# Optimization experiments

Hardware: AMD Instinct MI355X
Metric: run time of the kernel (lower is better)

The kernel has to match this reference:

```python
import jax, jax.numpy as jnp
import numpy as np

EPS = 1e-5  # torch GroupNorm default


def setup_inputs() -> dict:
    key = jax.random.key(0)
    ks = jax.random.split(key, 7)
    B, H, W, C = 8, 64, 64, 64
    x = jax.random.normal(ks[0], (B, H, W, C), dtype=jnp.float32)
    temb = jax.random.normal(ks[1], (B, 256), dtype=jnp.float32)
    scale = 0.02
    Wq = jax.random.normal(ks[2], (C, C), dtype=jnp.float32) * scale
    Wk = jax.random.normal(ks[3], (C, C), dtype=jnp.float32) * scale
    Wv = jax.random.normal(ks[4], (C, C), dtype=jnp.float32) * scale
    Wo = jax.random.normal(ks[5], (C, C), dtype=jnp.float32) * scale
    z = jnp.zeros((C,), dtype=jnp.float32)
    return {"x": x, "temb": temb, "Wq": Wq, "bq": z, "Wk": Wk, "bk": z,
            "Wv": Wv, "bv": z, "Wo": Wo, "bo": z}


def reference(x, temb, Wq, bq, Wk, bk, Wv, bv, Wo, bo):
    # x: [B, H, W, C] channels-last. temb is accepted but unused (as in source).
    B, H, W, C = x.shape
    S = H * W
    # normalize(): freshly-built GroupNorm(num_groups=1) with identity affine
    # -> standardize over all non-batch dims.
    mu = jnp.mean(x, axis=(1, 2, 3), keepdims=True)
    var = jnp.var(x, axis=(1, 2, 3), keepdims=True)
    h = (x - mu) * jax.lax.rsqrt(var + EPS)
    hf = h.reshape(B, S, C)
    q = hf @ Wq.T + bq  # [B, S, C]
    k = hf @ Wk.T + bk
    v = hf @ Wv.T + bv
    # full (S x S) score matrix, scaled by C^-0.5, naive softmax
    w = jnp.einsum('bsc,btc->bst', q, k) * (C ** -0.5)
    w = jax.nn.softmax(w, axis=-1)
    o = jnp.einsum('bst,btc->bsc', w, v)  # [B, S, C]
    o = o @ Wo.T + bo
    return x + o.reshape(B, H, W, C)
```

## Files before the change

### kernel.cpp

```cpp
#include <hip/hip_runtime.h>
#include <hip/hip_bf16.h>
#include <math.h>

#define B_ 8
#define S_ 4096
#define C_ 64
#define EPSV 1e-5f

using floatx4  = __attribute__((ext_vector_type(4)))  float;
using floatx16 = __attribute__((ext_vector_type(16))) float;
using bf16x8   = __attribute__((ext_vector_type(8)))  short;

typedef __attribute__((address_space(3))) unsigned int       as3_u32;
typedef __attribute__((address_space(1))) const unsigned int as1_u32;

__device__ __forceinline__ short f2bf(float f) {
    unsigned u = __builtin_bit_cast(unsigned, f);
    u = u + 0x7fffu + ((u >> 16) & 1u);
    return (short)(u >> 16);
}

__device__ __forceinline__ float bf2f(short s) {
    return __builtin_bit_cast(float, ((unsigned)(unsigned short)s) << 16);
}

__device__ __forceinline__ unsigned cvt_pk_bf16(float lo, float hi) {
    unsigned r;
    asm volatile("v_cvt_pk_bf16_f32 %0, %1, %2" : "=v"(r) : "v"(lo), "v"(hi));
    return r;
}

__device__ __forceinline__ void perm32swap(unsigned &a, unsigned &b) {
#if __has_builtin(__builtin_amdgcn_permlane32_swap)
    auto r = __builtin_amdgcn_permlane32_swap((int)a, (int)b, false, false);
    a = (unsigned)r[0];
    b = (unsigned)r[1];
#else
    asm volatile("v_permlane32_swap_b32 %0, %1" : "+v"(a), "+v"(b));
#endif
}

__device__ __forceinline__ bf16x8 ld_w_frag(const float* __restrict__ W, int n, int kk, int g, int c) {
    const float* p = W + (16 * n + c) * C_ + 32 * kk + 8 * g;
    bf16x8 r;
#pragma unroll
    for (int j = 0; j < 8; ++j) r[j] = f2bf(p[j]);
    return r;
}

__global__ __launch_bounds__(256) void stats1_kernel(const float* __restrict__ x,
                                                     float* __restrict__ partial) {
    int b = blockIdx.x >> 5, chunk = blockIdx.x & 31;
    const float4* xb = (const float4*)x + (size_t)b * 65536 + chunk * 2048;
    float s = 0.f, ss = 0.f;
#pragma unroll
    for (int i = 0; i < 8; ++i) {
        float4 v = xb[threadIdx.x + i * 256];
        s  += v.x + v.y + v.z + v.w;
        ss += v.x * v.x + v.y * v.y + v.z * v.z + v.w * v.w;
    }
    for (int off = 32; off > 0; off >>= 1) {
        s  += __shfl_down(s, off);
        ss += __shfl_down(ss, off);
    }
    __shared__ float sm[4], ssm[4];
    int wid = threadIdx.x >> 6, lane = threadIdx.x & 63;
    if (lane == 0) { sm[wid] = s; ssm[wid] = ss; }
    __syncthreads();
    if (threadIdx.x == 0) {
        partial[blockIdx.x * 2]     = sm[0] + sm[1] + sm[2] + sm[3];
        partial[blockIdx.x * 2 + 1] = ssm[0] + ssm[1] + ssm[2] + ssm[3];
    }
}

__global__ __launch_bounds__(512) void stats2_kernel(const float* __restrict__ partial,
                                                     float* __restrict__ stats) {
    int w = threadIdx.x >> 6, lane = threadIdx.x & 63;
    float s = 0.f, ss = 0.f;
    if (lane < 32) {
        s  = partial[(w * 32 + lane) * 2];
        ss = partial[(w * 32 + lane) * 2 + 1];
    }
    for (int off = 16; off > 0; off >>= 1) {
        s  += __shfl_down(s, off);
        ss += __shfl_down(ss, off);
    }
    if (lane == 0) {
        const float invN = 1.0f / (float)(S_ * C_);
        float mu  = s * invN;
        float var = ss * invN - mu * mu;
        stats[w * 2]     = mu;
        stats[w * 2 + 1] = rsqrtf(var + EPSV);
    }
}

__global__ __launch_bounds__(256) void proj_kernel(
    const float* __restrict__ x,
    const float* __restrict__ Wq, const float* __restrict__ bq,
    const float* __restrict__ Wk, const float* __restrict__ bk,
    const float* __restrict__ Wv, const float* __restrict__ bv,
    const float* __restrict__ stats,
    short* __restrict__ qo, char* __restrict__ kws, char* __restrict__ vws) {
    __shared__ char hbuf[64 * 128];

    int b  = blockIdx.x >> 6;
    int t_ = blockIdx.x & 63;
    int s0 = t_ * 64;
    float mu = stats[b * 2], rs = stats[b * 2 + 1];
    const float* xt = x + ((size_t)b * S_ + s0) * C_;
    int t = threadIdx.x;

#pragma unroll
    for (int i = 0; i < 4; ++i) {
        int fi  = t + 256 * i;
        int row = fi >> 4;
        int c4  = fi & 15;
        float4 v = *(const float4*)(xt + row * C_ + c4 * 4);
        unsigned lo = (unsigned)(unsigned short)f2bf((v.x - mu) * rs) |
                      ((unsigned)(unsigned short)f2bf((v.y - mu) * rs) << 16);
        unsigned hi = (unsigned)(unsigned short)f2bf((v.z - mu) * rs) |
                      ((unsigned)(unsigned short)f2bf((v.w - mu) * rs) << 16);
        int off = row * 128 + c4 * 8;
        off ^= (row & 7) << 4;
        *(uint2*)(hbuf + off) = make_uint2(lo, hi);
    }
    __syncthreads();

    int lane = t & 63, w = t >> 6;
    int g = lane >> 4, c = lane & 15;

    auto ld_h = [&](int row, int kcol) -> bf16x8 {
        int off = row * 128 + kcol * 2;
        off ^= (row & 7) << 4;
        return *(const bf16x8*)(hbuf + off);
    };

    bf16x8 ha[2];
    ha[0] = ld_h(16 * w + c, 8 * g);
    ha[1] = ld_h(16 * w + c, 32 + 8 * g);

    const float QSC = 0.125f * 1.44269504088896340736f;

#pragma unroll
    for (int n = 0; n < 4; ++n) {
        floatx4 aq = {0.f, 0.f, 0.f, 0.f}, ak = {0.f, 0.f, 0.f, 0.f};
#pragma unroll
        for (int kk = 0; kk < 2; ++kk) {
            bf16x8 wq = ld_w_frag(Wq, n, kk, g, c);
            bf16x8 wk = ld_w_frag(Wk, n, kk, g, c);
            aq = __builtin_amdgcn_mfma_f32_16x16x32_bf16(ha[kk], wq, aq, 0, 0, 0);
            ak = __builtin_amdgcn_mfma_f32_16x16x32_bf16(ha[kk], wk, ak, 0, 0, 0);
        }
        float bqv = bq[16 * n + c], bkv = bk[16 * n + c];
#pragma unroll
        for (int r = 0; r < 4; ++r) {
            int rr = 16 * w + 4 * g + r;
            qo[((size_t)b * S_ + s0 + rr) * C_ + 16 * n + c] = f2bf((aq[r] + bqv) * QSC);
            int r32 = rr & 31;
            size_t tb = ((size_t)b * 128 + 2 * t_ + (rr >> 5)) * 4096;
            int koff = (r32 * 128 + (16 * n + c) * 2) ^ ((r32 & 7) << 4);
            *(short*)(kws + tb + koff) = f2bf(ak[r] + bkv);
        }
    }

    bf16x8 wv[2];
    wv[0] = ld_w_frag(Wv, w, 0, g, c);
    wv[1] = ld_w_frag(Wv, w, 1, g, c);
    float bvr[4];
#pragma unroll
    for (int r = 0; r < 4; ++r) bvr[r] = bv[16 * w + 4 * g + r];

#pragma unroll
    for (int n = 0; n < 4; ++n) {
        floatx4 av = {0.f, 0.f, 0.f, 0.f};
#pragma unroll
        for (int kk = 0; kk < 2; ++kk) {
            bf16x8 hb = ld_h(16 * n + c, 32 * kk + 8 * g);
            av = __builtin_amdgcn_mfma_f32_16x16x32_bf16(wv[kk], hb, av, 0, 0, 0);
        }
        int u   = 16 * n + c;
        int u32 = u & 31;
        size_t tb = ((size_t)b * 128 + 2 * t_ + (u >> 5)) * 4096;
#pragma unroll
        for (int r = 0; r < 4; ++r) {
            int rr = 16 * w + 4 * g + r;
            int voff = (rr * 64 + u32 * 2) ^ (((rr >> 1) & 3) << 4);
            *(short*)(vws + tb + voff) = f2bf(av[r] + bvr[r]);
        }
    }
}

__global__ __launch_bounds__(256, 4) void flash_kernel(
    const short* __restrict__ qm, const char* __restrict__ kws, const char* __restrict__ vws,
    short* __restrict__ Opart, float2* __restrict__ mlpart) {
    __shared__ char lds[16384];

    int bid = blockIdx.x;
    int logical = (bid & 7) * 128 + (bid >> 3);
    int b = logical >> 7;
    int rest = logical & 127;
    int q0 = (rest >> 2) * 128;
    int quarter = rest & 3;
    int t = threadIdx.x;
    int lane = t & 63, w = t >> 6;
    int r5 = lane & 31, hi = lane >> 5;
    int qw = q0 + 32 * w;

    const char* kbase = kws + (size_t)b * 128 * 4096;
    const char* vbase = vws + (size_t)b * 128 * 4096;
    const short* qp = qm + (size_t)b * S_ * C_;

    bf16x8 bq[4];
#pragma unroll
    for (int kk = 0; kk < 4; ++kk)
        bq[kk] = *(const bf16x8*)(qp + (qw + r5) * C_ + 16 * kk + 8 * hi);

    floatx16 oacc[2];
#pragma unroll
    for (int mm = 0; mm < 2; ++mm)
#pragma unroll
        for (int i = 0; i < 16; ++i) oacc[mm][i] = 0.f;
    float m = -64.f, nm = 64.f, l = 0.f;

    const int kxm = (r5 & 7) << 4;
    const int vxm = ((r5 >> 1) & 3) << 4;

    auto STAGE = [&](int bi, int tt) {
        const char* gk = kbase + (size_t)tt * 4096 + t * 16;
        const char* gv = vbase + (size_t)tt * 4096 + t * 16;
        char* lk = lds +        bi * 4096 + t * 16;
        char* lv = lds + 8192 + bi * 4096 + t * 16;
        __builtin_amdgcn_global_load_lds((as1_u32*)gk, (as3_u32*)lk, 16, 0, 0);
        __builtin_amdgcn_global_load_lds((as1_u32*)gv, (as3_u32*)lv, 16, 0, 0);
    };

    auto ld_k = [&](const char* buf, int kk) -> bf16x8 {
        return *(const bf16x8*)(buf + r5 * 128 + ((32 * kk + 16 * hi) ^ kxm));
    };
    auto ld_v = [&](const char* buf, int mm, int s) -> bf16x8 {
        return *(const bf16x8*)(buf + (32 * mm + r5) * 64 + ((32 * s + 16 * hi) ^ vxm));
    };

    auto COMPUTE = [&](int bi) {
        const char* kbuf = lds +        bi * 4096;
        const char* vbuf = lds + 8192 + bi * 4096;
        floatx16 st;
#pragma unroll
        for (int i = 0; i < 16; ++i) st[i] = nm;
        __builtin_amdgcn_s_setprio(1);
#pragma unroll
        for (int kk = 0; kk < 4; ++kk) {
            bf16x8 ak = ld_k(kbuf, kk);
            st = __builtin_amdgcn_mfma_f32_32x32x16_bf16(ak, bq[kk], st, 0, 0, 0);
        }
        __builtin_amdgcn_s_setprio(0);
        bf16x8 av[2][2];
#pragma unroll
        for (int mm = 0; mm < 2; ++mm)
#pragma unroll
            for (int s = 0; s < 2; ++s)
                av[mm][s] = ld_v(vbuf, mm, s);
        float mt = st[0];
#pragma unroll
        for (int i = 1; i < 16; ++i) mt = fmaxf(mt, st[i]);
        mt = fmaxf(mt, __shfl_xor(mt, 32));
        if (!__all(mt <= 8.0f)) {
            float d = fmaxf(mt, 0.f);
            float a = __builtin_amdgcn_exp2f(-d);
            m += d;
            nm = -m;
            l *= a;
#pragma unroll
            for (int mm = 0; mm < 2; ++mm) oacc[mm] *= a;
#pragma unroll
            for (int i = 0; i < 16; ++i) st[i] -= d;
        }
        float e[16], psum = 0.f;
#pragma unroll
        for (int i = 0; i < 16; ++i) e[i] = __builtin_amdgcn_exp2f(st[i]);
#pragma unroll
        for (int i = 0; i < 16; ++i) psum += e[i];
        l += psum;
        unsigned wd[8];
#pragma unroll
        for (int j = 0; j < 8; ++j) wd[j] = cvt_pk_bf16(e[2 * j], e[2 * j + 1]);
        perm32swap(wd[0], wd[2]);
        perm32swap(wd[1], wd[3]);
        perm32swap(wd[4], wd[6]);
        perm32swap(wd[5], wd[7]);
        uint4 u0 = make_uint4(wd[0], wd[1], wd[2], wd[3]);
        uint4 u1 = make_uint4(wd[4], wd[5], wd[6], wd[7]);
        bf16x8 bp0 = __builtin_bit_cast(bf16x8, u0);
        bf16x8 bp1 = __builtin_bit_cast(bf16x8, u1);
        __builtin_amdgcn_s_setprio(1);
#pragma unroll
        for (int mm = 0; mm < 2; ++mm) {
            oacc[mm] = __builtin_amdgcn_mfma_f32_32x32x16_bf16(av[mm][0], bp0, oacc[mm], 0, 0, 0);
            oacc[mm] = __builtin_amdgcn_mfma_f32_32x32x16_bf16(av[mm][1], bp1, oacc[mm], 0, 0, 0);
        }
        __builtin_amdgcn_s_setprio(0);
    };

    const int base = quarter * 32;
    STAGE(0, base);
    __syncthreads();
    for (int r = 0; r < 32; r += 2) {
        STAGE(1, base + r + 1);
        COMPUTE(0);
        __syncthreads();
        if (r + 2 < 32) STAGE(0, base + r + 2);
        COMPUTE(1);
        __syncthreads();
    }

    l += __shfl_xor(l, 32);

    size_t prow = (size_t)(quarter * 8 + b) * S_ + q0;
    if (lane < 32)
        mlpart[prow + 32 * w + r5] = make_float2(m, l);

    short* op = Opart + (prow + 32 * w + r5) * C_;
#pragma unroll
    for (int mm = 0; mm < 2; ++mm) {
#pragma unroll
        for (int j = 0; j < 4; ++j) {
            int ch = 32 * mm + 8 * j + 4 * hi;
            uint2 u = make_uint2(cvt_pk_bf16(oacc[mm][4 * j],     oacc[mm][4 * j + 1]),
                                 cvt_pk_bf16(oacc[mm][4 * j + 2], oacc[mm][4 * j + 3]));
            *(uint2*)(op + ch) = u;
        }
    }
}

__global__ __launch_bounds__(256) void combine_kernel(
    const short* __restrict__ Opart, const float2* __restrict__ mlpart,
    const float* __restrict__ Wo, const float* __restrict__ bo,
    const float* __restrict__ x, float* __restrict__ out) {
    __shared__ char obuf[8192];

    int bid = blockIdx.x;
    int logical = (bid & 7) * 64 + (bid >> 3);
    int b = logical >> 6;
    int q0 = (logical & 63) * 64;
    int t = threadIdx.x;
    int lane = t & 63, w = t >> 6;
    int g = lane >> 4, c = lane & 15;

    const short*  P[4];
    const float2* ml[4];
#pragma unroll
    for (int h = 0; h < 4; ++h) {
        P[h]  = Opart  + ((size_t)(h * 8 + b) * S_ + q0) * C_;
        ml[h] = mlpart + (size_t)(h * 8 + b) * S_ + q0;
    }

#pragma unroll
    for (int i = 0; i < 16; ++i) {
        int idx = t + 256 * i;
        int q = idx >> 6, ch = idx & 63;
        float2 a0 = ml[0][q], a1 = ml[1][q], a2 = ml[2][q], a3 = ml[3][q];
        float M = fmaxf(fmaxf(a0.x, a1.x), fmaxf(a2.x, a3.x));
        float s0 = __builtin_amdgcn_exp2f(a0.x - M);
        float s1 = __builtin_amdgcn_exp2f(a1.x - M);
        float s2 = __builtin_amdgcn_exp2f(a2.x - M);
        float s3 = __builtin_amdgcn_exp2f(a3.x - M);
        float L  = a0.y * s0 + a1.y * s1 + a2.y * s2 + a3.y * s3;
        float o  = (bf2f(P[0][q * 64 + ch]) * s0 + bf2f(P[1][q * 64 + ch]) * s1 +
                    bf2f(P[2][q * 64 + ch]) * s2 + bf2f(P[3][q * 64 + ch]) * s3) / L;
        int off = (q * 128 + ch * 2) ^ ((q & 7) << 4);
        *(short*)(obuf + off) = f2bf(o);
    }
    __syncthreads();

    bf16x8 ao[2];
    {
        int row = 16 * w + c;
        int off0 = (row * 128 + (8 * g) * 2)      ^ ((row & 7) << 4);
        int off1 = (row * 128 + (32 + 8 * g) * 2) ^ ((row & 7) << 4);
        ao[0] = *(const bf16x8*)(obuf + off0);
        ao[1] = *(const bf16x8*)(obuf + off1);
    }
#pragma unroll
    for (int n = 0; n < 4; ++n) {
        floatx4 a = {0.f, 0.f, 0.f, 0.f};
#pragma unroll
        for (int kk = 0; kk < 2; ++kk) {
            bf16x8 bw = ld_w_frag(Wo, n, kk, g, c);
            a = __builtin_amdgcn_mfma_f32_16x16x32_bf16(ao[kk], bw, a, 0, 0, 0);
        }
        float bov = bo[16 * n + c];
#pragma unroll
        for (int r = 0; r < 4; ++r) {
            int srow = q0 + 16 * w + 4 * g + r;
            size_t idx = ((size_t)b * S_ + srow) * C_ + 16 * n + c;
            out[idx] = x[idx] + bov + a[r];
        }
    }
}

extern "C" void kernel_launch(void* const* d_in, const int* in_sizes, int n_in,
                              void* d_out, int out_size, void* d_ws, size_t ws_size,
                              hipStream_t stream) {
    const float* x  = (const float*)d_in[0];
    const float* Wq = (const float*)d_in[2];
    const float* bq = (const float*)d_in[3];
    const float* Wk = (const float*)d_in[4];
    const float* bk = (const float*)d_in[5];
    const float* Wv = (const float*)d_in[6];
    const float* bv = (const float*)d_in[7];
    const float* Wo = (const float*)d_in[8];
    const float* bo = (const float*)d_in[9];
    float* out = (float*)d_out;

    char* ws = (char*)d_ws;
    float*  partial = (float*)ws;
    float*  stats   = (float*)(ws + 2048);
    short*  q   = (short*)(ws + 4096);
    char*   kt  = (char*)(q + (size_t)B_ * S_ * C_);
    char*   vt  = kt + (size_t)B_ * 128 * 4096;
    short*  op  = (short*)(vt + (size_t)B_ * 128 * 4096);
    float2* mlp = (float2*)((char*)op + (size_t)4 * B_ * S_ * C_ * 2);

    stats1_kernel<<<256, 256, 0, stream>>>(x, partial);
    stats2_kernel<<<1, 512, 0, stream>>>(partial, stats);
    proj_kernel<<<B_ * (S_ / 64), 256, 0, stream>>>(x, Wq, bq, Wk, bk, Wv, bv, stats, q, kt, vt);
    flash_kernel<<<B_ * (S_ / 128) * 4, 256, 0, stream>>>(q, kt, vt, op, mlp);
    combine_kernel<<<B_ * (S_ / 64), 256, 0, stream>>>(op, mlp, Wo, bo, x, out);
}
```

Baseline: 80.69 us.

## Stage QKV projections in LDS for coalesced stores; speculative exp in flash softmax

```diff
diff --git a/kernel.cpp b/kernel.cpp
--- a/kernel.cpp
+++ b/kernel.cpp
@@ -101,7 +101,10 @@
     const float* __restrict__ Wv, const float* __restrict__ bv,
     const float* __restrict__ stats,
     short* __restrict__ qo, char* __restrict__ kws, char* __restrict__ vws) {
-    __shared__ char hbuf[64 * 128];
+    __shared__ char hbuf[8192];
+    __shared__ char qimg[8192];
+    __shared__ char kimg[8192];
+    __shared__ char vimg[8192];
 
     int b  = blockIdx.x >> 6;
     int t_ = blockIdx.x & 63;
@@ -155,11 +158,10 @@
 #pragma unroll
         for (int r = 0; r < 4; ++r) {
             int rr = 16 * w + 4 * g + r;
-            qo[((size_t)b * S_ + s0 + rr) * C_ + 16 * n + c] = f2bf((aq[r] + bqv) * QSC);
+            *(short*)(qimg + rr * 128 + (16 * n + c) * 2) = f2bf((aq[r] + bqv) * QSC);
             int r32 = rr & 31;
-            size_t tb = ((size_t)b * 128 + 2 * t_ + (rr >> 5)) * 4096;
             int koff = (r32 * 128 + (16 * n + c) * 2) ^ ((r32 & 7) << 4);
-            *(short*)(kws + tb + koff) = f2bf(ak[r] + bkv);
+            *(short*)(kimg + (rr >> 5) * 4096 + koff) = f2bf(ak[r] + bkv);
         }
     }
 
@@ -180,13 +182,22 @@
         }
         int u   = 16 * n + c;
         int u32 = u & 31;
-        size_t tb = ((size_t)b * 128 + 2 * t_ + (u >> 5)) * 4096;
 #pragma unroll
         for (int r = 0; r < 4; ++r) {
             int rr = 16 * w + 4 * g + r;
             int voff = (rr * 64 + u32 * 2) ^ (((rr >> 1) & 3) << 4);
-            *(short*)(vws + tb + voff) = f2bf(av[r] + bvr[r]);
-        }
+            *(short*)(vimg + (u >> 5) * 4096 + voff) = f2bf(av[r] + bvr[r]);
+        }
+    }
+    __syncthreads();
+
+    size_t gb = ((size_t)b * 128 + 2 * t_) * 4096;
+    uint4* qdst = (uint4*)(qo + ((size_t)b * S_ + s0) * C_);
+#pragma unroll
+    for (int i = 0; i < 2; ++i) {
+        qdst[t + 256 * i] = *(const uint4*)(qimg + i * 4096 + t * 16);
+        *(uint4*)(kws + gb + i * 4096 + t * 16) = *(const uint4*)(kimg + i * 4096 + t * 16);
+        *(uint4*)(vws + gb + i * 4096 + t * 16) = *(const uint4*)(vimg + i * 4096 + t * 16);
     }
 }
 
@@ -220,7 +231,10 @@
     for (int mm = 0; mm < 2; ++mm)
 #pragma unroll
         for (int i = 0; i < 16; ++i) oacc[mm][i] = 0.f;
-    float m = -64.f, nm = 64.f, l = 0.f;
+    float m = -64.f, l = 0.f;
+    floatx16 nmv;
+#pragma unroll
+    for (int i = 0; i < 16; ++i) nmv[i] = 64.f;
 
     const int kxm = (r5 & 7) << 4;
     const int vxm = ((r5 >> 1) & 3) << 4;
@@ -244,15 +258,11 @@
     auto COMPUTE = [&](int bi) {
         const char* kbuf = lds +        bi * 4096;
         const char* vbuf = lds + 8192 + bi * 4096;
-        floatx16 st;
-#pragma unroll
-        for (int i = 0; i < 16; ++i) st[i] = nm;
         __builtin_amdgcn_s_setprio(1);
-#pragma unroll
-        for (int kk = 0; kk < 4; ++kk) {
-            bf16x8 ak = ld_k(kbuf, kk);
-            st = __builtin_amdgcn_mfma_f32_32x32x16_bf16(ak, bq[kk], st, 0, 0, 0);
-        }
+        floatx16 st = __builtin_amdgcn_mfma_f32_32x32x16_bf16(ld_k(kbuf, 0), bq[0], nmv, 0, 0, 0);
+#pragma unroll
+        for (int kk = 1; kk < 4; ++kk)
+            st = __builtin_amdgcn_mfma_f32_32x32x16_bf16(ld_k(kbuf, kk), bq[kk], st, 0, 0, 0);
         __builtin_amdgcn_s_setprio(0);
         bf16x8 av[2][2];
 #pragma unroll
@@ -260,26 +270,30 @@
 #pragma unroll
             for (int s = 0; s < 2; ++s)
                 av[mm][s] = ld_v(vbuf, mm, s);
-        float mt = st[0];
-#pragma unroll
-        for (int i = 1; i < 16; ++i) mt = fmaxf(mt, st[i]);
-        mt = fmaxf(mt, __shfl_xor(mt, 32));
-        if (!__all(mt <= 8.0f)) {
+        float e[16], psum;
+#pragma unroll
+        for (int i = 0; i < 16; ++i) e[i] = __builtin_amdgcn_exp2f(st[i]);
+        psum = ((e[0] + e[1]) + (e[2] + e[3])) + ((e[4] + e[5]) + (e[6] + e[7])) +
+               ((e[8] + e[9]) + (e[10] + e[11])) + ((e[12] + e[13]) + (e[14] + e[15]));
+        if (!__all(psum <= 1.0e18f)) {
+            float mt = fmaxf(fmaxf(fmaxf(st[0], st[1]), fmaxf(st[2], st[3])),
+                             fmaxf(fmaxf(st[4], st[5]), fmaxf(st[6], st[7])));
+            mt = fmaxf(mt, fmaxf(fmaxf(fmaxf(st[8], st[9]), fmaxf(st[10], st[11])),
+                                 fmaxf(fmaxf(st[12], st[13]), fmaxf(st[14], st[15]))));
+            mt = fmaxf(mt, __shfl_xor(mt, 32));
             float d = fmaxf(mt, 0.f);
             float a = __builtin_amdgcn_exp2f(-d);
             m += d;
-            nm = -m;
             l *= a;
 #pragma unroll
             for (int mm = 0; mm < 2; ++mm) oacc[mm] *= a;
 #pragma unroll
-            for (int i = 0; i < 16; ++i) st[i] -= d;
-        }
-        float e[16], psum = 0.f;
-#pragma unroll
-        for (int i = 0; i < 16; ++i) e[i] = __builtin_amdgcn_exp2f(st[i]);
-#pragma unroll
-        for (int i = 0; i < 16; ++i) psum += e[i];
+            for (int i = 0; i < 16; ++i) { st[i] -= d; nmv[i] = -m; }
+#pragma unroll
+            for (int i = 0; i < 16; ++i) e[i] = __builtin_amdgcn_exp2f(st[i]);
+            psum = ((e[0] + e[1]) + (e[2] + e[3])) + ((e[4] + e[5]) + (e[6] + e[7])) +
+                   ((e[8] + e[9]) + (e[10] + e[11])) + ((e[12] + e[13]) + (e[14] + e[15]));
+        }
         l += psum;
         unsigned wd[8];
 #pragma unroll
```

Measured after the change: 123.0 us. 1.52x slower.
